# Kernel tuning notes

Hardware: AMD Instinct MI355X
Metric: run time of the kernel (lower is better)

The kernel has to match this reference:

```python
import jax, jax.numpy as jnp
import numpy as np

MODEL_SIZE = 1024
H = 16
KEY_SIZE = MODEL_SIZE // H


def setup_inputs() -> dict:
    key = jax.random.key(0)
    ks = jax.random.split(key, 10)
    B, SQ, SK, D = 2, 2048, 2048, MODEL_SIZE
    s = 1.0 / np.sqrt(D)
    return {
        "decoder_output": jax.random.normal(ks[0], (B, SQ, D), jnp.float32),
        "encoder_output": jax.random.normal(ks[1], (B, SK, D), jnp.float32),
        "wq": jax.random.normal(ks[2], (D, D), jnp.float32) * s,
        "bq": jnp.zeros((D,), jnp.float32),
        "wk": jax.random.normal(ks[3], (D, D), jnp.float32) * s,
        "bk": jnp.zeros((D,), jnp.float32),
        "wv": jax.random.normal(ks[4], (D, D), jnp.float32) * s,
        "bv": jnp.zeros((D,), jnp.float32),
        "wo": jax.random.normal(ks[5], (D, D), jnp.float32) * s,
        "bo": jnp.zeros((D,), jnp.float32),
    }


def reference(decoder_output, encoder_output, wq, bq, wk, bk, wv, bv, wo, bo):
    B, SQ, D = decoder_output.shape
    SK = encoder_output.shape[1]
    # QKV projections (Dense = x @ W + b)
    q = decoder_output @ wq + bq          # [B, SQ, D]
    k = encoder_output @ wk + bk          # [B, SK, D]
    v = encoder_output @ wv + bv          # [B, SK, D]
    # split heads -> [B, H, S, key_size]
    q = q.reshape(B, SQ, H, KEY_SIZE).transpose(0, 2, 1, 3)
    k = k.reshape(B, SK, H, KEY_SIZE).transpose(0, 2, 1, 3)
    v = v.reshape(B, SK, H, KEY_SIZE).transpose(0, 2, 1, 3)
    scale = 1.0 / jnp.sqrt(jnp.asarray(KEY_SIZE, q.dtype))
    score = jnp.einsum('bhqd,bhkd->bhqk', q, k) * scale   # [B, H, SQ, SK]
    align = jax.nn.softmax(score, axis=-1)
    ctx = jnp.einsum('bhqk,bhkd->bhqd', align, v)          # [B, H, SQ, key_size]
    ctx = ctx.transpose(0, 2, 1, 3).reshape(B, SQ, D)
    return ctx @ wo + bo
```

## Files before the change

kernel.cpp:

```cpp
#include <hip/hip_runtime.h>
#include <hip/hip_fp16.h>

typedef __attribute__((ext_vector_type(8))) _Float16 f16x8;
typedef __attribute__((ext_vector_type(4))) _Float16 f16x4;
typedef __attribute__((ext_vector_type(4))) float    f32x4;

#define MFMA_F16(a,b,c) __builtin_amdgcn_mfma_f32_16x16x32_f16((a),(b),(c),0,0,0)
#define GL16(s_, d_) __builtin_amdgcn_global_load_lds((const __attribute__((address_space(1))) void*)(s_), \
                       (__attribute__((address_space(3))) void*)(d_), 16, 0, 0)


__global__ __launch_bounds__(256) void k_cast(const float* __restrict__ dec, const float* __restrict__ enc,
                                              _Float16* __restrict__ dd, _Float16* __restrict__ de)
{
  int i = blockIdx.x * 256 + threadIdx.x;
  float4 a = ((const float4*)dec)[i];
  float4 b = ((const float4*)enc)[i];
  f16x4 ha = {(_Float16)a.x, (_Float16)a.y, (_Float16)a.z, (_Float16)a.w};
  f16x4 hb = {(_Float16)b.x, (_Float16)b.y, (_Float16)b.z, (_Float16)b.w};
  ((f16x4*)dd)[i] = ha;
  ((f16x4*)de)[i] = hb;
}

__global__ __launch_bounds__(256) void k_wt(const float* __restrict__ wq, const float* __restrict__ wk,
                                            const float* __restrict__ wv, const float* __restrict__ wo,
                                            _Float16* __restrict__ dst0)
{
  __shared__ float tile[32][33];
  int z = blockIdx.z;
  const float* w = (z==0)?wq:(z==1)?wk:(z==2)?wv:wo;
  _Float16* dst = dst0 + (size_t)z * (1024u*1024u);
  int tx = threadIdx.x, ty = threadIdx.y;
  int n0 = blockIdx.x*32, k0 = blockIdx.y*32;
#pragma unroll
  for (int r = 0; r < 4; ++r)
    tile[ty + 8*r][tx] = w[(size_t)(k0 + ty + 8*r)*1024 + n0 + tx];
  __syncthreads();
#pragma unroll
  for (int r = 0; r < 4; ++r)
    dst[(size_t)(n0 + ty + 8*r)*1024 + k0 + tx] = (_Float16)tile[tx][ty + 8*r];
}

__device__ __forceinline__ void gemm_core_128(const _Float16* __restrict__ A, const _Float16* __restrict__ BT,
                                              int m0, int n0, _Float16* lds, f32x4 acc[4][4])
{
  const int t    = threadIdx.x;
  const int lane = t & 63;
  const int wid  = t >> 6;
  const int lr   = lane & 15, lg = lane >> 4;
  const int wm   = (wid & 1) * 64, wn = (wid >> 1) * 64;
  const int swz  = (lr >> 2) & 3;

  const int cm0 = t >> 2,         ck0 = (((t      ) & 3) ^ (((t      ) >> 4) & 3)) * 8;
  const int cm1 = (t + 256) >> 2, ck1 = (((t + 256) & 3) ^ (((t + 256) >> 4) & 3)) * 8;
  const _Float16* Arow0 = A  + (size_t)(m0 + cm0) * 1024 + ck0;
  const _Float16* Arow1 = A  + (size_t)(m0 + cm1) * 1024 + ck1;
  const _Float16* Brow0 = BT + (size_t)(n0 + cm0) * 1024 + ck0;
  const _Float16* Brow1 = BT + (size_t)(n0 + cm1) * 1024 + ck1;

  _Float16* l0 = lds + t*8;
  _Float16* l1 = lds + (t+256)*8;
  _Float16* l2 = lds + 4096 + t*8;
  _Float16* l3 = lds + 4096 + (t+256)*8;

#define STAGE_GL(buf_, ko_) { GL16(Arow0+(ko_), l0+(buf_)*8192); GL16(Arow1+(ko_), l1+(buf_)*8192); \
                              GL16(Brow0+(ko_), l2+(buf_)*8192); GL16(Brow1+(ko_), l3+(buf_)*8192); }

  int aoff[4], boff[4];
#pragma unroll
  for (int s = 0; s < 4; ++s) {
    aoff[s] = (wm + s*16 + lr)*32 + ((lg ^ swz) << 3);
    boff[s] = (wn + s*16 + lr)*32 + ((lg ^ swz) << 3);
  }

  const f32x4 z4 = {0.f,0.f,0.f,0.f};
#pragma unroll
  for (int i = 0; i < 4; ++i)
#pragma unroll
    for (int j = 0; j < 4; ++j) acc[i][j] = z4;

  STAGE_GL(0, 0);
  __syncthreads();

  int cur = 0;
#pragma unroll 1
  for (int kt = 0; kt < 32; ++kt) {
    if (kt < 31) STAGE_GL(cur ^ 1, (kt + 1) * 32);
    const _Float16* la = lds + cur * 8192;
    const _Float16* lb = la + 4096;
    f16x8 af[4], bf[4];
#pragma unroll
    for (int s = 0; s < 4; ++s) af[s] = *(const f16x8*)(la + aoff[s]);
#pragma unroll
    for (int s = 0; s < 4; ++s) bf[s] = *(const f16x8*)(lb + boff[s]);
#pragma unroll
    for (int i = 0; i < 4; ++i)
#pragma unroll
      for (int j = 0; j < 4; ++j)
        acc[i][j] = MFMA_F16(af[i], bf[j], acc[i][j]);
    __syncthreads();
    cur ^= 1;
  }
#undef STAGE_GL
}

__global__ __launch_bounds__(256, 2) void k_qkv(const _Float16* __restrict__ dec16, const _Float16* __restrict__ enc16,
                                                const _Float16* __restrict__ wT,
                                                const float* __restrict__ bq, const float* __restrict__ bk,
                                                const float* __restrict__ bv,
                                                _Float16* __restrict__ Qo, _Float16* __restrict__ Ko,
                                                _Float16* __restrict__ Vt)
{
  __shared__ _Float16 lds[16384];
  const int z = blockIdx.z;
  const _Float16* A    = (z == 0) ? dec16 : enc16;
  const _Float16* BT   = wT + (size_t)z * (1024u*1024u);
  const float*    bias = (z == 0) ? bq : (z == 1) ? bk : bv;

  const int bx = blockIdx.x;
  const int m0 = (bx >> 3) * 128, n0 = (bx & 7) * 128;
  const int lane = threadIdx.x & 63, wid = threadIdx.x >> 6;
  const int lr = lane & 15, lg = lane >> 4;
  const int wm = (wid & 1) * 64, wn = (wid >> 1) * 64;

  f32x4 acc[4][4];
  gemm_core_128(A, BT, m0, n0, lds, acc);

  if (z < 2) {
    _Float16* dst = (z == 0) ? Qo : Ko;
#pragma unroll
    for (int i = 0; i < 4; ++i)
#pragma unroll
      for (int j = 0; j < 4; ++j) {
        int n = n0 + wn + j*16 + lr;
        int h = n >> 6, d = n & 63;
        float bb = bias[n];
        f32x4 v = acc[i][j];
#pragma unroll
        for (int r = 0; r < 4; ++r) {
          int m = m0 + wm + i*16 + 4*lg + r;
          int b = m >> 11, s = m & 2047;
          dst[((size_t)(b*16 + h)*2048 + s)*64 + d] = (_Float16)(v[r] + bb);
        }
      }
  } else {
#pragma unroll
    for (int i = 0; i < 4; ++i)
#pragma unroll
      for (int j = 0; j < 4; ++j) {
        int n = n0 + wn + j*16 + lr;
        int h = n >> 6, d = n & 63;
        float bb = bias[n];
        int m = m0 + wm + i*16 + 4*lg;
        int b = m >> 11, s = m & 2047;
        int sp = (s & ~31) | (((s >> 2) & 3) << 3) | (((s >> 4) & 1) << 2);
        f16x4 pv = {(_Float16)(acc[i][j][0] + bb), (_Float16)(acc[i][j][1] + bb),
                    (_Float16)(acc[i][j][2] + bb), (_Float16)(acc[i][j][3] + bb)};
        *(f16x4*)&Vt[((size_t)(b*16 + h)*64 + d)*2048 + sp] = pv;
      }
  }
}

__global__ __launch_bounds__(256, 2) void k_out(const _Float16* __restrict__ ctx, const _Float16* __restrict__ woT,
                                                const float* __restrict__ bo, float* __restrict__ out)
{
  __shared__ _Float16 lds[16384];
  const int bx = blockIdx.x;
  const int m0 = (bx >> 3) * 128, n0 = (bx & 7) * 128;
  const int lane = threadIdx.x & 63, wid = threadIdx.x >> 6;
  const int lr = lane & 15, lg = lane >> 4;
  const int wm = (wid & 1) * 64, wn = (wid >> 1) * 64;

  f32x4 acc[4][4];
  gemm_core_128(ctx, woT, m0, n0, lds, acc);

#pragma unroll
  for (int i = 0; i < 4; ++i)
#pragma unroll
    for (int j = 0; j < 4; ++j) {
      int n = n0 + wn + j*16 + lr;
      float bb = bo[n];
#pragma unroll
      for (int r = 0; r < 4; ++r) {
        int m = m0 + wm + i*16 + 4*lg + r;
        out[(size_t)m*1024 + n] = acc[i][j][r] + bb;
      }
    }
}

__global__ __launch_bounds__(256, 2) void k_attn(const _Float16* __restrict__ Q, const _Float16* __restrict__ K,
                                                 const _Float16* __restrict__ Vt, _Float16* __restrict__ ctx)
{
  __shared__ _Float16 lds[16384];
  const int bid  = blockIdx.x;
  const int xcd  = bid & 7, slot = bid >> 3;
  const int bh   = xcd*4 + (slot >> 4);
  const int qt   = slot & 15;
  const int t    = threadIdx.x;
  const int wid  = t >> 6, lane = t & 63;
  const int lr   = lane & 15, lg = lane >> 4;
  const int qbase = qt*128 + wid*32;

  const _Float16* Qp = Q  + ((size_t)bh*2048 + qbase)*64;
  const _Float16* Kp = K  + (size_t)bh*2048*64;
  const _Float16* Vp = Vt + (size_t)bh*64*2048;

  const float ALPHA = 0.125f * 1.44269504f;
  const f32x4 z4 = {0.f,0.f,0.f,0.f};

  const int c1  = t + 256;
  const int kr0 = t  >> 3, lc0 = ((t  & 7) ^ (kr0 & 7)) * 8;
  const int kr1 = c1 >> 3, lc1 = ((c1 & 7) ^ (kr1 & 7)) * 8;
  const _Float16* Ks0 = Kp + (size_t)kr0*64   + lc0;
  const _Float16* Ks1 = Kp + (size_t)kr1*64   + lc1;
  const _Float16* Vs0 = Vp + (size_t)kr0*2048 + lc0;
  const _Float16* Vs1 = Vp + (size_t)kr1*2048 + lc1;
  _Float16* lK0 = lds + t*8;
  _Float16* lK1 = lds + c1*8;
  _Float16* lV0 = lds + 4096 + t*8;
  _Float16* lV1 = lds + 4096 + c1*8;

#define STAGE(buf_, kt_) { GL16(Ks0 + (size_t)(kt_)*4096, lK0 + (buf_)*8192); \
                           GL16(Ks1 + (size_t)(kt_)*4096, lK1 + (buf_)*8192); \
                           GL16(Vs0 + (kt_)*64,           lV0 + (buf_)*8192); \
                           GL16(Vs1 + (kt_)*64,           lV1 + (buf_)*8192); }

  f16x8 qf[2][2];
#pragma unroll
  for (int qs = 0; qs < 2; ++qs)
#pragma unroll
    for (int d2 = 0; d2 < 2; ++d2)
      qf[qs][d2] = *(const f16x8*)&Qp[(size_t)(qs*16 + lr)*64 + d2*32 + 8*lg];

  f32x4 acc[4][2];
#pragma unroll
  for (int dt = 0; dt < 4; ++dt) { acc[dt][0] = z4; acc[dt][1] = z4; }
  float lrun[2] = {0.f, 0.f};

  const int kswz = lr & 7;

  STAGE(0, 0);
  __syncthreads();

  int cur = 0;
#pragma unroll 1
  for (int kt = 0; kt < 32; ++kt) {
    if (kt < 31) STAGE(cur ^ 1, kt + 1);
    const _Float16* bK = lds + cur*8192;
    const _Float16* bV = bK + 4096;
#pragma unroll
    for (int ks2 = 0; ks2 < 2; ++ks2) {
      f16x8 kf[2][2], vf[4];
#pragma unroll
      for (int ks = 0; ks < 2; ++ks)
#pragma unroll
        for (int d2 = 0; d2 < 2; ++d2)
          kf[ks][d2] = *(const f16x8*)&bK[(ks2*32 + ks*16 + lr)*64 + ((((d2<<2)|lg) ^ kswz) << 3)];
#pragma unroll
      for (int dt = 0; dt < 4; ++dt)
        vf[dt] = *(const f16x8*)&bV[(dt*16 + lr)*64 + ((((ks2<<2)|lg) ^ kswz) << 3)];

      f32x4 st[2][2];
      __builtin_amdgcn_s_setprio(1);
#pragma unroll
      for (int ks = 0; ks < 2; ++ks)
#pragma unroll
        for (int qs = 0; qs < 2; ++qs) {
          f32x4 s_ = MFMA_F16(kf[ks][0], qf[qs][0], z4);
          st[ks][qs] = MFMA_F16(kf[ks][1], qf[qs][1], s_);
        }
      __builtin_amdgcn_s_setprio(0);
      f16x8 pt[2];
#pragma unroll
      for (int qs = 0; qs < 2; ++qs) {
        float pv[8];
#pragma unroll
        for (int i = 0; i < 4; ++i) { pv[i] = st[0][qs][i]; pv[4+i] = st[1][qs][i]; }
        float ssum = 0.f;
        f16x8 ptv;
#pragma unroll
        for (int i = 0; i < 8; ++i) {
          float e = exp2f(pv[i] * ALPHA);
          ssum += e;
          ptv[i] = (_Float16)e;
        }
        lrun[qs] += ssum;
        pt[qs] = ptv;
      }
      __builtin_amdgcn_s_setprio(1);
#pragma unroll
      for (int dt = 0; dt < 4; ++dt)
#pragma unroll
        for (int qs = 0; qs < 2; ++qs)
          acc[dt][qs] = MFMA_F16(vf[dt], pt[qs], acc[dt][qs]);
      __builtin_amdgcn_s_setprio(0);
    }
    __syncthreads();
    cur ^= 1;
  }

#pragma unroll
  for (int qs = 0; qs < 2; ++qs) {
    float L = lrun[qs];
    L += __shfl_xor(L, 16);
    L += __shfl_xor(L, 32);
    float inv = 1.f / L;
    int q = qbase + qs*16 + lr;
    _Float16* cp = ctx + ((size_t)((bh >> 4)*2048 + q))*1024 + (bh & 15)*64;
#pragma unroll
    for (int dt = 0; dt < 4; ++dt) {
      f16x4 o = {(_Float16)(acc[dt][qs][0]*inv), (_Float16)(acc[dt][qs][1]*inv),
                 (_Float16)(acc[dt][qs][2]*inv), (_Float16)(acc[dt][qs][3]*inv)};
      *(f16x4*)&cp[dt*16 + 4*lg] = o;
    }
  }
#undef STAGE
}

extern "C" void kernel_launch(void* const* d_in, const int* in_sizes, int n_in,
                              void* d_out, int out_size, void* d_ws, size_t ws_size,
                              hipStream_t stream) {
  const float* dec = (const float*)d_in[0];
  const float* enc = (const float*)d_in[1];
  const float* wq  = (const float*)d_in[2];
  const float* bq  = (const float*)d_in[3];
  const float* wk  = (const float*)d_in[4];
  const float* bk  = (const float*)d_in[5];
  const float* wv  = (const float*)d_in[6];
  const float* bv  = (const float*)d_in[7];
  const float* wo  = (const float*)d_in[8];
  const float* bo  = (const float*)d_in[9];

  char* ws = (char*)d_ws;
  _Float16* dec16 = (_Float16*)(ws + (0ull  << 20));
  _Float16* enc16 = (_Float16*)(ws + (8ull  << 20));
  _Float16* wT    = (_Float16*)(ws + (16ull << 20));
  _Float16* Qh    = (_Float16*)(ws + (24ull << 20));
  _Float16* Kh    = (_Float16*)(ws + (32ull << 20));
  _Float16* Vt    = (_Float16*)(ws + (40ull << 20));
  _Float16* ctx   = (_Float16*)(ws + (48ull << 20));
  float* out = (float*)d_out;

  k_cast<<<4096, 256, 0, stream>>>(dec, enc, dec16, enc16);
  k_wt<<<dim3(32, 32, 4), dim3(32, 8), 0, stream>>>(wq, wk, wv, wo, wT);
  k_qkv<<<dim3(256, 1, 3), 256, 0, stream>>>(dec16, enc16, wT, bq, bk, bv, Qh, Kh, Vt);
  k_attn<<<512, 256, 0, stream>>>(Qh, Kh, Vt, ctx);
  k_out<<<256, 256, 0, stream>>>(ctx, wT + 3ull*1024*1024, bo, out);
}
```

Before: 219.4 us.

## Triple-buffer GEMM loads, remap blocks per XCD, fold softmax scale into Q

The shared GEMM core moves from a double-buffered loop to a three-stage LDS ring. Loads are issued two tiles ahead and waited on with explicit vmcnt counts plus a single raw barrier per iteration, replacing two __syncthreads. The QKV and output GEMMs use a flattened grid with an XCD-aware block remap and allow 3 blocks per CU, which needs 48KB of LDS per block. The softmax scale times log2(e) is now applied when Q is written, removing a multiply per score in attention at the cost of scaling Q before its fp16 rounding.

After: 211.1 us. -3.8%, faster.

```diff
diff --git a/kernel.cpp b/kernel.cpp
--- a/kernel.cpp
+++ b/kernel.cpp
@@ -80,12 +80,15 @@
     for (int j = 0; j < 4; ++j) acc[i][j] = z4;
 
   STAGE_GL(0, 0);
-  __syncthreads();
+  STAGE_GL(1, 32);
 
   int cur = 0;
 #pragma unroll 1
   for (int kt = 0; kt < 32; ++kt) {
-    if (kt < 31) STAGE_GL(cur ^ 1, (kt + 1) * 32);
+    if (kt < 31) { asm volatile("s_waitcnt vmcnt(4)" ::: "memory"); }
+    else         { asm volatile("s_waitcnt vmcnt(0)" ::: "memory"); }
+    __builtin_amdgcn_s_barrier();
+    __builtin_amdgcn_sched_barrier(0);
     const _Float16* la = lds + cur * 8192;
     const _Float16* lb = la + 4096;
     f16x8 af[4], bf[4];
@@ -98,36 +101,43 @@
 #pragma unroll
       for (int j = 0; j < 4; ++j)
         acc[i][j] = MFMA_F16(af[i], bf[j], acc[i][j]);
-    __syncthreads();
-    cur ^= 1;
+    if (kt < 30) {
+      int nx = cur + 2; if (nx >= 3) nx -= 3;
+      STAGE_GL(nx, (kt + 2) * 32);
+    }
+    cur = (cur + 1 == 3) ? 0 : cur + 1;
   }
 #undef STAGE_GL
 }
 
-__global__ __launch_bounds__(256, 2) void k_qkv(const _Float16* __restrict__ dec16, const _Float16* __restrict__ enc16,
+__global__ __launch_bounds__(256, 3) void k_qkv(const _Float16* __restrict__ dec16, const _Float16* __restrict__ enc16,
                                                 const _Float16* __restrict__ wT,
                                                 const float* __restrict__ bq, const float* __restrict__ bk,
                                                 const float* __restrict__ bv,
                                                 _Float16* __restrict__ Qo, _Float16* __restrict__ Ko,
                                                 _Float16* __restrict__ Vt)
 {
-  __shared__ _Float16 lds[16384];
-  const int z = blockIdx.z;
+  __shared__ _Float16 lds[24576];
+  const int lin = blockIdx.x;
+  const int b768 = (lin & 7) * 96 + (lin >> 3);
+  const int z  = b768 >> 8;
+  const int bx = b768 & 255;
   const _Float16* A    = (z == 0) ? dec16 : enc16;
   const _Float16* BT   = wT + (size_t)z * (1024u*1024u);
   const float*    bias = (z == 0) ? bq : (z == 1) ? bk : bv;
 
-  const int bx = blockIdx.x;
   const int m0 = (bx >> 3) * 128, n0 = (bx & 7) * 128;
   const int lane = threadIdx.x & 63, wid = threadIdx.x >> 6;
   const int lr = lane & 15, lg = lane >> 4;
   const int wm = (wid & 1) * 64, wn = (wid >> 1) * 64;
+  const float QSCL = 0.125f * 1.44269504f;
 
   f32x4 acc[4][4];
   gemm_core_128(A, BT, m0, n0, lds, acc);
 
   if (z < 2) {
     _Float16* dst = (z == 0) ? Qo : Ko;
+    const float scl = (z == 0) ? QSCL : 1.0f;
 #pragma unroll
     for (int i = 0; i < 4; ++i)
 #pragma unroll
@@ -140,7 +150,7 @@
         for (int r = 0; r < 4; ++r) {
           int m = m0 + wm + i*16 + 4*lg + r;
           int b = m >> 11, s = m & 2047;
-          dst[((size_t)(b*16 + h)*2048 + s)*64 + d] = (_Float16)(v[r] + bb);
+          dst[((size_t)(b*16 + h)*2048 + s)*64 + d] = (_Float16)((v[r] + bb) * scl);
         }
       }
   } else {
@@ -161,11 +171,12 @@
   }
 }
 
-__global__ __launch_bounds__(256, 2) void k_out(const _Float16* __restrict__ ctx, const _Float16* __restrict__ woT,
+__global__ __launch_bounds__(256, 3) void k_out(const _Float16* __restrict__ ctx, const _Float16* __restrict__ woT,
                                                 const float* __restrict__ bo, float* __restrict__ out)
 {
-  __shared__ _Float16 lds[16384];
-  const int bx = blockIdx.x;
+  __shared__ _Float16 lds[24576];
+  const int lin = blockIdx.x;
+  const int bx = (lin & 7) * 32 + (lin >> 3);
   const int m0 = (bx >> 3) * 128, n0 = (bx & 7) * 128;
   const int lane = threadIdx.x & 63, wid = threadIdx.x >> 6;
   const int lr = lane & 15, lg = lane >> 4;
@@ -205,7 +216,6 @@
   const _Float16* Kp = K  + (size_t)bh*2048*64;
   const _Float16* Vp = Vt + (size_t)bh*64*2048;
 
-  const float ALPHA = 0.125f * 1.44269504f;
   const f32x4 z4 = {0.f,0.f,0.f,0.f};
 
   const int c1  = t + 256;
@@ -280,7 +290,7 @@
         f16x8 ptv;
 #pragma unroll
         for (int i = 0; i < 8; ++i) {
-          float e = exp2f(pv[i] * ALPHA);
+          float e = exp2f(pv[i]);
           ssum += e;
           ptv[i] = (_Float16)e;
         }
@@ -343,7 +353,7 @@
 
   k_cast<<<4096, 256, 0, stream>>>(dec, enc, dec16, enc16);
   k_wt<<<dim3(32, 32, 4), dim3(32, 8), 0, stream>>>(wq, wk, wv, wo, wT);
-  k_qkv<<<dim3(256, 1, 3), 256, 0, stream>>>(dec16, enc16, wT, bq, bk, bv, Qh, Kh, Vt);
+  k_qkv<<<768, 256, 0, stream>>>(dec16, enc16, wT, bq, bk, bv, Qh, Kh, Vt);
   k_attn<<<512, 256, 0, stream>>>(Qh, Kh, Vt, ctx);
   k_out<<<256, 256, 0, stream>>>(ctx, wT + 3ull*1024*1024, bo, out);
 }
```
